# Performance work log

Hardware: AMD Instinct MI355X
Metric: run time of the kernel (lower is better)

The kernel has to match this reference:

```python
import jax, jax.numpy as jnp
import numpy as np

B, N, L, H = 8, 2048, 1280, 160
GAMMA = 1.0  # fixed buffer, gamma_init_value=1, not trainable


def setup_inputs() -> dict:
    key = jax.random.key(0)
    ks = jax.random.split(key, 7)
    s_in = 1.0 / np.sqrt(L)  # conv1d default init scale (approx; randn used for testing)
    return {
        "x": jax.random.normal(ks[0], (B, N, L), dtype=jnp.float32),
        "Wq": jax.random.normal(ks[1], (H, L), dtype=jnp.float32) * s_in,
        "bq": jax.random.normal(ks[2], (H,), dtype=jnp.float32) * s_in,
        "Wk": jax.random.normal(ks[3], (H, L), dtype=jnp.float32) * s_in,
        "bk": jax.random.normal(ks[4], (H,), dtype=jnp.float32) * s_in,
        "Wv": jax.random.normal(ks[5], (L, L), dtype=jnp.float32) * s_in,
        "bv": jax.random.normal(ks[6], (L,), dtype=jnp.float32) * s_in,
    }


def reference(x, Wq, bq, Wk, bk, Wv, bv):
    # 1x1 Conv1d on x.permute(0,2,1) == per-token linear projection
    q = jnp.einsum("bnl,hl->bnh", x, Wq) + bq          # [B,N,H]
    k = jnp.einsum("bnl,hl->bnh", x, Wk) + bk          # [B,N,H]
    v = jnp.einsum("bnl,ml->bnm", x, Wv) + bv          # [B,N,L]
    energy = jnp.einsum("bih,bjh->bij", q, k)          # [B,N,N]
    attn = jax.nn.softmax(energy, axis=-1)
    out = jnp.einsum("bij,bjm->bim", attn, v)          # [B,N,L]
    return GAMMA * out + x                              # [B,N,L]
```

## Files before the change

kernel.cpp:

```cpp
#include <hip/hip_runtime.h>

#define BB 8
#define NN 2048
#define LL 1280
#define HH 160
#define BN (BB*NN)
#define NO (2*HH + LL)
#define SHIFT 40.0f

typedef __attribute__((ext_vector_type(8))) short short8;
typedef __attribute__((ext_vector_type(4))) float floatx4;

__device__ __forceinline__ unsigned short f2bf(float f) {
    unsigned int u = __builtin_bit_cast(unsigned int, f);
    u = (u + 0x7FFFu + ((u >> 16) & 1u)) >> 16;
    return (unsigned short)u;
}
__device__ __forceinline__ float bf2f(unsigned short h) {
    unsigned int u = ((unsigned int)h) << 16;
    return __builtin_bit_cast(float, u);
}
__device__ __forceinline__ void split2(float f, unsigned short& hi, unsigned short& lo) {
    hi = f2bf(f);
    lo = f2bf(f - bf2f(hi));
}


__device__ __forceinline__ void gl16(const unsigned short* g, unsigned short* l) {
    __builtin_amdgcn_global_load_lds(
        (const __attribute__((address_space(1))) unsigned int*)g,
        (__attribute__((address_space(3))) unsigned int*)l, 16, 0, 0);
}

__global__ __launch_bounds__(256) void cast_w(
    const float* __restrict__ Wq, const float* __restrict__ Wk, const float* __restrict__ Wv,
    unsigned short* __restrict__ wqk_h, unsigned short* __restrict__ wqk_l,
    unsigned short* __restrict__ wv)
{
    int o = blockIdx.x;
    if (o < 2*HH) {
        const float* src = (o < HH) ? (Wq + (size_t)o * LL) : (Wk + (size_t)(o - HH) * LL);
        unsigned short* dh = wqk_h + (size_t)o * LL;
        unsigned short* dl = wqk_l + (size_t)o * LL;
        for (int c = threadIdx.x; c < LL; c += 256) {
            unsigned short h, l;
            split2(src[c], h, l);
            dh[c] = h; dl[c] = l;
        }
    } else {
        int f = o - 2*HH;
        const float* src = Wv + (size_t)f * LL;
        unsigned short* dstF = wv + (size_t)(f >> 4) * 20480 + (f & 15) * 8;
        for (int c = threadIdx.x * 4; c < LL; c += 256 * 4) {
            float4 v = *(const float4*)(src + c);
            ushort4 u;
            u.x = f2bf(v.x); u.y = f2bf(v.y); u.z = f2bf(v.z); u.w = f2bf(v.w);
            *(ushort4*)(dstF + (size_t)(c >> 5) * 512 + ((c >> 3) & 3) * 128 + (c & 7)) = u;
        }
    }
}

__global__ __launch_bounds__(256) void cast_x(
    const float* __restrict__ x, unsigned short* __restrict__ xh)
{
    const int g   = blockIdx.x;
    const int tid = threadIdx.x;
    const float* src = x + (size_t)(g * 16 + (tid & 15)) * LL + ((tid >> 4) & 3) * 8;
    unsigned short* dst = xh + (size_t)g * 20480 + tid * 8;
    const int ks0 = tid >> 6;
    #pragma unroll
    for (int it = 0; it < 10; it++) {
        int k0 = (it * 4 + ks0) * 32;
        float4 f0 = *(const float4*)(src + k0);
        float4 f1 = *(const float4*)(src + k0 + 4);
        short8 h8;
        h8[0]=(short)f2bf(f0.x); h8[1]=(short)f2bf(f0.y); h8[2]=(short)f2bf(f0.z); h8[3]=(short)f2bf(f0.w);
        h8[4]=(short)f2bf(f1.x); h8[5]=(short)f2bf(f1.y); h8[6]=(short)f2bf(f1.z); h8[7]=(short)f2bf(f1.w);
        *(short8*)(dst + it * 2048) = h8;
    }
}

__global__ __launch_bounds__(256, 2) void proj_qk(
    const float* __restrict__ x,
    const unsigned short* __restrict__ wh, const unsigned short* __restrict__ wl,
    const float* __restrict__ bq, const float* __restrict__ bk,
    unsigned short* __restrict__ qh, unsigned short* __restrict__ ql,
    unsigned short* __restrict__ kh, unsigned short* __restrict__ kl)
{
    __shared__ __align__(16) unsigned short Ah[128 * 40];
    __shared__ __align__(16) unsigned short Al[128 * 40];
    __shared__ __align__(16) unsigned short Bh[64 * 40];
    __shared__ __align__(16) unsigned short Bl[64 * 40];

    const int o0 = blockIdx.x * 64;
    const int m0 = blockIdx.y * 128;
    const int tid = threadIdx.x;
    const int wave = tid >> 6, lane = tid & 63;
    const int l15 = lane & 15, l4 = lane >> 4;

    floatx4 acc[2][4] = {};

    const int sr = tid >> 2;
    const int sc = (tid & 3) * 8;

    for (int k0 = 0; k0 < LL; k0 += 32) {
        __syncthreads();
        #pragma unroll
        for (int h = 0; h < 2; h++) {
            int r = sr + h * 64;
            const float* xp = x + (size_t)(m0 + r) * LL + k0 + sc;
            float4 f0 = *(const float4*)xp;
            float4 f1 = *(const float4*)(xp + 4);
            float fv[8] = {f0.x, f0.y, f0.z, f0.w, f1.x, f1.y, f1.z, f1.w};
            short8 h8, l8;
            #pragma unroll
            for (int i = 0; i < 8; i++) {
                unsigned short hh, lll;
                split2(fv[i], hh, lll);
                h8[i] = (short)hh; l8[i] = (short)lll;
            }
            *(short8*)&Ah[r * 40 + sc] = h8;
            *(short8*)&Al[r * 40 + sc] = l8;
        }
        *(short8*)&Bh[sr * 40 + sc] = *(const short8*)&wh[(size_t)(o0 + sr) * LL + k0 + sc];
        *(short8*)&Bl[sr * 40 + sc] = *(const short8*)&wl[(size_t)(o0 + sr) * LL + k0 + sc];
        __syncthreads();

        short8 ah0 = *(const short8*)&Ah[(wave * 32 + l15) * 40 + l4 * 8];
        short8 ah1 = *(const short8*)&Ah[(wave * 32 + 16 + l15) * 40 + l4 * 8];
        short8 al0 = *(const short8*)&Al[(wave * 32 + l15) * 40 + l4 * 8];
        short8 al1 = *(const short8*)&Al[(wave * 32 + 16 + l15) * 40 + l4 * 8];
        #pragma unroll
        for (int ct = 0; ct < 4; ct++) {
            short8 bh8 = *(const short8*)&Bh[(ct * 16 + l15) * 40 + l4 * 8];
            short8 bl8 = *(const short8*)&Bl[(ct * 16 + l15) * 40 + l4 * 8];
            acc[0][ct] = __builtin_amdgcn_mfma_f32_16x16x32_bf16(ah0, bh8, acc[0][ct], 0, 0, 0);
            acc[0][ct] = __builtin_amdgcn_mfma_f32_16x16x32_bf16(al0, bh8, acc[0][ct], 0, 0, 0);
            acc[0][ct] = __builtin_amdgcn_mfma_f32_16x16x32_bf16(ah0, bl8, acc[0][ct], 0, 0, 0);
            acc[1][ct] = __builtin_amdgcn_mfma_f32_16x16x32_bf16(ah1, bh8, acc[1][ct], 0, 0, 0);
            acc[1][ct] = __builtin_amdgcn_mfma_f32_16x16x32_bf16(al1, bh8, acc[1][ct], 0, 0, 0);
            acc[1][ct] = __builtin_amdgcn_mfma_f32_16x16x32_bf16(ah1, bl8, acc[1][ct], 0, 0, 0);
        }
    }

    #pragma unroll
    for (int rt = 0; rt < 2; rt++)
        #pragma unroll
        for (int ct = 0; ct < 4; ct++)
            #pragma unroll
            for (int r = 0; r < 4; r++) {
                int m = m0 + wave * 32 + rt * 16 + l4 * 4 + r;
                int o = o0 + ct * 16 + l15;
                float val = acc[rt][ct][r] + ((o < HH) ? bq[o] : bk[o - HH]);
                unsigned short vh, vl;
                split2(val, vh, vl);
                int oo = (o < HH) ? o : (o - HH);
                size_t fa = (size_t)(m >> 4) * 2560 + (oo >> 5) * 512
                          + ((oo >> 3) & 3) * 128 + (m & 15) * 8 + (oo & 7);
                if (o < HH) {
                    qh[fa] = vh;
                    ql[fa] = vl;
                } else {
                    kh[fa] = vh;
                    kl[fa] = vl;
                }
            }
}

__global__ __launch_bounds__(256, 3) void proj_v(
    const unsigned short* __restrict__ xh, const unsigned short* __restrict__ wv,
    const float* __restrict__ bv, unsigned short* __restrict__ vt)
{
    __shared__ __align__(16) unsigned short Sm[3 * 8192];

    const int bid = blockIdx.x;
    const int xcd = bid & 7;
    const int q   = bid >> 3;
    const int mt  = xcd * 16 + q / 10;
    const int ft  = q % 10;
    const int m0 = mt * 128;
    const int f0 = ft * 128;

    const int tid = threadIdx.x;
    const int wave = tid >> 6, lane = tid & 63;
    const int l15 = lane & 15, l4 = lane >> 4;
    const int wm = wave >> 1, wn = wave & 1;

    const unsigned short* AF = xh + (size_t)(m0 >> 4) * 20480;
    const unsigned short* BF = wv + (size_t)(f0 >> 4) * 20480;

    const int sp0 = tid, sp1 = 256 + tid;
    const unsigned sa0 = (unsigned)(sp0 >> 6) * 20480u + (sp0 & 63) * 8;
    const unsigned sa1 = (unsigned)(sp1 >> 6) * 20480u + (sp1 & 63) * 8;

    floatx4 acc[4][4] = {};

    auto STAGE = [&](int slot, int ks) {
        unsigned short* A  = Sm + slot * 8192;
        unsigned short* Bs = A + 4096;
        const unsigned ko = (unsigned)ks * 512u;
        gl16(AF + sa0 + ko, A  + sp0 * 8);
        gl16(BF + sa0 + ko, Bs + sp0 * 8);
        gl16(AF + sa1 + ko, A  + sp1 * 8);
        gl16(BF + sa1 + ko, Bs + sp1 * 8);
    };

    auto COMPUTE = [&](int slot) {
        const unsigned short* A  = Sm + slot * 8192;
        const unsigned short* Bs = A + 4096;
        short8 a[4], bb[4];
        #pragma unroll
        for (int mf = 0; mf < 4; mf++)
            a[mf] = *(const short8*)(A + ((wm * 4 + mf) * 64 + lane) * 8);
        #pragma unroll
        for (int nf = 0; nf < 4; nf++)
            bb[nf] = *(const short8*)(Bs + ((wn * 4 + nf) * 64 + lane) * 8);
        __builtin_amdgcn_s_setprio(1);
        #pragma unroll
        for (int mf = 0; mf < 4; mf++)
            #pragma unroll
            for (int nf = 0; nf < 4; nf++)
                acc[mf][nf] = __builtin_amdgcn_mfma_f32_16x16x32_bf16(a[mf], bb[nf], acc[mf][nf], 0, 0, 0);
        __builtin_amdgcn_s_setprio(0);
    };

    STAGE(0, 0); STAGE(1, 1); STAGE(2, 2);

    int s = 0;
    for (int kt = 0; kt < 37; ++kt) {
        asm volatile("s_waitcnt vmcnt(8)" ::: "memory");
        asm volatile("s_barrier" ::: "memory");
        COMPUTE(s);
        asm volatile("s_barrier" ::: "memory");
        STAGE(s, kt + 3);
        s = (s == 2) ? 0 : s + 1;
    }
    asm volatile("s_waitcnt vmcnt(8)" ::: "memory");
    asm volatile("s_barrier" ::: "memory");
    COMPUTE(s); s = (s == 2) ? 0 : s + 1;
    asm volatile("s_waitcnt vmcnt(4)" ::: "memory");
    asm volatile("s_barrier" ::: "memory");
    COMPUTE(s); s = (s == 2) ? 0 : s + 1;
    asm volatile("s_waitcnt vmcnt(0)" ::: "memory");
    asm volatile("s_barrier" ::: "memory");
    COMPUTE(s);

    const int b    = m0 >> 11;
    const int tokb = (m0 & 2047) + wm * 64;
    unsigned short* vtB = vt + (size_t)b * LL * NN;
    float bvv[4];
    #pragma unroll
    for (int nf = 0; nf < 4; nf++)
        bvv[nf] = bv[f0 + wn * 64 + nf * 16 + l15];

    #pragma unroll
    for (int mf = 0; mf < 4; mf++)
        #pragma unroll
        for (int nf = 0; nf < 4; nf++) {
            int f   = f0 + wn * 64 + nf * 16 + l15;
            int tok = tokb + mf * 16 + l4 * 4;
            ushort4 u;
            u.x = f2bf(acc[mf][nf][0] + bvv[nf]);
            u.y = f2bf(acc[mf][nf][1] + bvv[nf]);
            u.z = f2bf(acc[mf][nf][2] + bvv[nf]);
            u.w = f2bf(acc[mf][nf][3] + bvv[nf]);
            *(ushort4*)(vtB + (size_t)(f >> 4) * 32768 + (tok >> 5) * 512
                        + ((tok >> 3) & 3) * 128 + (f & 15) * 8 + (tok & 7)) = u;
        }
}

__global__ __launch_bounds__(256, 2) void s_exp(
    const unsigned short* __restrict__ qhp, const unsigned short* __restrict__ qlp,
    const unsigned short* __restrict__ khp, const unsigned short* __restrict__ klp,
    unsigned short* __restrict__ P, float* __restrict__ Lsum)
{
    __shared__ float sums[4][32];
    const int b  = blockIdx.y;
    const int i0 = blockIdx.x * 32;
    const int tid = threadIdx.x;
    const int wave = tid >> 6, lane = tid & 63;
    const int l15 = lane & 15, l4 = lane >> 4;

    short8 aqh[2][5], aql[2][5];
    #pragma unroll
    for (int rt = 0; rt < 2; rt++) {
        const size_t rowb = (size_t)((b * NN + i0 + rt * 16) >> 4) * 2560 + lane * 8;
        #pragma unroll
        for (int ks = 0; ks < 5; ks++) {
            aqh[rt][ks] = *(const short8*)&qhp[rowb + ks * 512];
            aql[rt][ks] = *(const short8*)&qlp[rowb + ks * 512];
        }
    }

    float sr[2][4] = {};
    unsigned short* Pb = P + (size_t)b * NN * NN + (size_t)(i0 >> 4) * 32768;

    for (int c0 = 0; c0 < NN; c0 += 256) {
        const int jb = c0 + wave * 64;
        #pragma unroll
        for (int ct = 0; ct < 4; ct++) {
            const int tok0 = jb + ct * 16;
            const int tok  = tok0 + l15;
            const size_t kbase = (size_t)((b * NN + tok0) >> 4) * 2560 + lane * 8;
            floatx4 a0[3] = {{0,0,0,0},{0,0,0,0},{0,0,0,0}};
            floatx4 a1[3] = {{0,0,0,0},{0,0,0,0},{0,0,0,0}};
            #pragma unroll
            for (int ks = 0; ks < 5; ks++) {
                short8 bh = *(const short8*)&khp[kbase + ks * 512];
                short8 bl = *(const short8*)&klp[kbase + ks * 512];
                a0[0] = __builtin_amdgcn_mfma_f32_16x16x32_bf16(aqh[0][ks], bh, a0[0], 0, 0, 0);
                a0[1] = __builtin_amdgcn_mfma_f32_16x16x32_bf16(aql[0][ks], bh, a0[1], 0, 0, 0);
                a0[2] = __builtin_amdgcn_mfma_f32_16x16x32_bf16(aqh[0][ks], bl, a0[2], 0, 0, 0);
                a1[0] = __builtin_amdgcn_mfma_f32_16x16x32_bf16(aqh[1][ks], bh, a1[0], 0, 0, 0);
                a1[1] = __builtin_amdgcn_mfma_f32_16x16x32_bf16(aql[1][ks], bh, a1[1], 0, 0, 0);
                a1[2] = __builtin_amdgcn_mfma_f32_16x16x32_bf16(aqh[1][ks], bl, a1[2], 0, 0, 0);
            }
            const size_t tbase = (size_t)(tok >> 5) * 512 + ((tok >> 3) & 3) * 128 + (tok & 7);
            #pragma unroll
            for (int r = 0; r < 4; r++) {
                float e0 = a0[0][r] + a0[1][r] + a0[2][r];
                float e1 = a1[0][r] + a1[1][r] + a1[2][r];
                unsigned short pb0 = f2bf(__expf(e0 - SHIFT));
                unsigned short pb1 = f2bf(__expf(e1 - SHIFT));
                Pb[tbase + (l4 * 4 + r) * 8] = pb0;
                Pb[tbase + (l4 * 4 + r) * 8 + 32768] = pb1;
                sr[0][r] += bf2f(pb0);
                sr[1][r] += bf2f(pb1);
            }
        }
    }

    #pragma unroll
    for (int rt = 0; rt < 2; rt++)
        #pragma unroll
        for (int r = 0; r < 4; r++) {
            float v = sr[rt][r];
            v += __shfl_xor(v, 1);
            v += __shfl_xor(v, 2);
            v += __shfl_xor(v, 4);
            v += __shfl_xor(v, 8);
            if (l15 == 0) sums[wave][rt * 16 + l4 * 4 + r] = v;
        }
    __syncthreads();
    if (tid < 32)
        Lsum[(size_t)b * NN + i0 + tid] =
            sums[0][tid] + sums[1][tid] + sums[2][tid] + sums[3][tid];
}

__global__ __launch_bounds__(256, 3) void pv_gemm(
    const unsigned short* __restrict__ P, const unsigned short* __restrict__ vt,
    const float* __restrict__ Lsum,
    const float* __restrict__ x, float* __restrict__ out)
{
    __shared__ __align__(16) unsigned short Sm[3 * 8192];

    const int p0 = blockIdx.x;
    const int b  = p0 & 7;
    const int t  = p0 >> 3;
    const int n0 = (t % 10) * 128;
    const int m0 = (t / 10) * 128;

    const int tid = threadIdx.x;
    const int wave = tid >> 6, lane = tid & 63;
    const int l15 = lane & 15, l4 = lane >> 4;
    const int wm = wave >> 1, wn = wave & 1;

    const unsigned short* PbF = P  + (size_t)b * NN * NN + (size_t)(m0 >> 4) * 32768;
    const unsigned short* VbF = vt + (size_t)b * LL * NN + (size_t)(n0 >> 4) * 32768;

    const int sp0 = tid, sp1 = 256 + tid;
    const unsigned sa0 = (unsigned)(sp0 >> 6) * 32768u + (sp0 & 63) * 8;
    const unsigned sa1 = (unsigned)(sp1 >> 6) * 32768u + (sp1 & 63) * 8;

    floatx4 acc[4][4] = {};

    auto STAGE = [&](int slot, int ks) {
        unsigned short* A  = Sm + slot * 8192;
        unsigned short* Bs = A + 4096;
        const unsigned ko = (unsigned)ks * 512u;
        gl16(PbF + sa0 + ko, A  + sp0 * 8);
        gl16(VbF + sa0 + ko, Bs + sp0 * 8);
        gl16(PbF + sa1 + ko, A  + sp1 * 8);
        gl16(VbF + sa1 + ko, Bs + sp1 * 8);
    };

    auto COMPUTE = [&](int slot) {
        const unsigned short* A  = Sm + slot * 8192;
        const unsigned short* Bs = A + 4096;
        short8 a[4], bb[4];
        #pragma unroll
        for (int mf = 0; mf < 4; mf++)
            a[mf] = *(const short8*)(A + ((wm * 4 + mf) * 64 + lane) * 8);
        #pragma unroll
        for (int nf = 0; nf < 4; nf++)
            bb[nf] = *(const short8*)(Bs + ((wn * 4 + nf) * 64 + lane) * 8);
        __builtin_amdgcn_s_setprio(1);
        #pragma unroll
        for (int mf = 0; mf < 4; mf++)
            #pragma unroll
            for (int nf = 0; nf < 4; nf++)
                acc[mf][nf] = __builtin_amdgcn_mfma_f32_16x16x32_bf16(a[mf], bb[nf], acc[mf][nf], 0, 0, 0);
        __builtin_amdgcn_s_setprio(0);
    };

    STAGE(0, 0); STAGE(1, 1); STAGE(2, 2);

    int s = 0;
    for (int kt = 0; kt < 61; ++kt) {
        asm volatile("s_waitcnt vmcnt(8)" ::: "memory");
        asm volatile("s_barrier" ::: "memory");
        COMPUTE(s);
        asm volatile("s_barrier" ::: "memory");
        STAGE(s, kt + 3);
        s = (s == 2) ? 0 : s + 1;
    }
    asm volatile("s_waitcnt vmcnt(8)" ::: "memory");
    asm volatile("s_barrier" ::: "memory");
    COMPUTE(s); s = (s == 2) ? 0 : s + 1;
    asm volatile("s_waitcnt vmcnt(4)" ::: "memory");
    asm volatile("s_barrier" ::: "memory");
    COMPUTE(s); s = (s == 2) ? 0 : s + 1;
    asm volatile("s_waitcnt vmcnt(0)" ::: "memory");
    asm volatile("s_barrier" ::: "memory");
    COMPUTE(s);

    float linv[4][4];
    #pragma unroll
    for (int mf = 0; mf < 4; mf++)
        #pragma unroll
        for (int r = 0; r < 4; r++)
            linv[mf][r] = 1.0f / Lsum[(size_t)b * NN + m0 + wm * 64 + mf * 16 + l4 * 4 + r];

    #pragma unroll
    for (int mf = 0; mf < 4; mf++)
        #pragma unroll
        for (int nf = 0; nf < 4; nf++)
            #pragma unroll
            for (int r = 0; r < 4; r++) {
                int row = m0 + wm * 64 + mf * 16 + l4 * 4 + r;
                int col = n0 + wn * 64 + nf * 16 + l15;
                size_t idx = ((size_t)b * NN + row) * LL + col;
                out[idx] = acc[mf][nf][r] * linv[mf][r] + x[idx];
            }
}

extern "C" void kernel_launch(void* const* d_in, const int* in_sizes, int n_in,
                              void* d_out, int out_size, void* d_ws, size_t ws_size,
                              hipStream_t stream) {
    const float* x  = (const float*)d_in[0];
    const float* Wq = (const float*)d_in[1];
    const float* bq = (const float*)d_in[2];
    const float* Wk = (const float*)d_in[3];
    const float* bk = (const float*)d_in[4];
    const float* Wv = (const float*)d_in[5];
    const float* bv = (const float*)d_in[6];
    float* out = (float*)d_out;

    unsigned short* wqk_h = (unsigned short*)d_ws;
    unsigned short* wqk_l = wqk_h + (size_t)2*HH * LL;
    unsigned short* wv    = wqk_l + (size_t)2*HH * LL;
    unsigned short* qh    = wv    + (size_t)LL * LL;
    unsigned short* ql    = qh    + (size_t)BN * HH;
    unsigned short* kh    = ql    + (size_t)BN * HH;
    unsigned short* kl    = kh    + (size_t)BN * HH;
    unsigned short* vt    = kl    + (size_t)BN * HH;
    unsigned short* P     = vt    + (size_t)BB * LL * NN;
    float*          Lsum  = (float*)(P + (size_t)BB * NN * NN);
    unsigned short* xh    = P;

    cast_w<<<dim3(NO), dim3(256), 0, stream>>>(Wq, Wk, Wv, wqk_h, wqk_l, wv);

    cast_x<<<dim3(BN / 16), dim3(256), 0, stream>>>(x, xh);

    dim3 gqk(2*HH / 64, BN / 128);
    proj_qk<<<gqk, dim3(256), 0, stream>>>(x, wqk_h, wqk_l, bq, bk, qh, ql, kh, kl);

    proj_v<<<dim3(1280), dim3(256), 0, stream>>>(xh, wv, bv, vt);

    dim3 gs(NN / 32, BB);
    s_exp<<<gs, dim3(256), 0, stream>>>(qh, ql, kh, kl, P, Lsum);

    pv_gemm<<<dim3(1280), dim3(256), 0, stream>>>(P, vt, Lsum, x, out);
}
```

Measured before the change: 479.2 us.

## Precompute x hi/lo bf16 split and restructure QK projection without LDS

cast_x now writes both the high and low bf16 parts of x in MFMA fragment layout, into a buffer that aliases vt. cast_w writes the Wq/Wk hi/lo parts in the same fragment layout. proj_qk is rewritten so each block covers 64 rows against all 320 Q/K outputs, loading fragments straight from global memory with no LDS staging or barriers. This removes the old behaviour of re-reading fp32 x and redoing the hi/lo split once per 64-column output block. The cost is an extra xl buffer write and every wave re-reading the shared A fragments from cache.

```diff
diff --git a/kernel.cpp b/kernel.cpp
--- a/kernel.cpp
+++ b/kernel.cpp
@@ -40,12 +40,13 @@
     int o = blockIdx.x;
     if (o < 2*HH) {
         const float* src = (o < HH) ? (Wq + (size_t)o * LL) : (Wk + (size_t)(o - HH) * LL);
-        unsigned short* dh = wqk_h + (size_t)o * LL;
-        unsigned short* dl = wqk_l + (size_t)o * LL;
+        unsigned short* dh = wqk_h + (size_t)(o >> 4) * 20480 + (o & 15) * 8;
+        unsigned short* dl = wqk_l + (size_t)(o >> 4) * 20480 + (o & 15) * 8;
         for (int c = threadIdx.x; c < LL; c += 256) {
             unsigned short h, l;
             split2(src[c], h, l);
-            dh[c] = h; dl[c] = l;
+            unsigned off = (unsigned)(c >> 5) * 512 + ((c >> 3) & 3) * 128 + (c & 7);
+            dh[off] = h; dl[off] = l;
         }
     } else {
         int f = o - 2*HH;
@@ -61,110 +62,96 @@
 }
 
 __global__ __launch_bounds__(256) void cast_x(
-    const float* __restrict__ x, unsigned short* __restrict__ xh)
+    const float* __restrict__ x,
+    unsigned short* __restrict__ xh, unsigned short* __restrict__ xl)
 {
     const int g   = blockIdx.x;
     const int tid = threadIdx.x;
     const float* src = x + (size_t)(g * 16 + (tid & 15)) * LL + ((tid >> 4) & 3) * 8;
-    unsigned short* dst = xh + (size_t)g * 20480 + tid * 8;
+    unsigned short* dsth = xh + (size_t)g * 20480 + tid * 8;
+    unsigned short* dstl = xl + (size_t)g * 20480 + tid * 8;
     const int ks0 = tid >> 6;
     #pragma unroll
     for (int it = 0; it < 10; it++) {
         int k0 = (it * 4 + ks0) * 32;
         float4 f0 = *(const float4*)(src + k0);
         float4 f1 = *(const float4*)(src + k0 + 4);
-        short8 h8;
-        h8[0]=(short)f2bf(f0.x); h8[1]=(short)f2bf(f0.y); h8[2]=(short)f2bf(f0.z); h8[3]=(short)f2bf(f0.w);
-        h8[4]=(short)f2bf(f1.x); h8[5]=(short)f2bf(f1.y); h8[6]=(short)f2bf(f1.z); h8[7]=(short)f2bf(f1.w);
-        *(short8*)(dst + it * 2048) = h8;
+        float fv[8] = {f0.x, f0.y, f0.z, f0.w, f1.x, f1.y, f1.z, f1.w};
+        short8 h8, l8;
+        #pragma unroll
+        for (int i = 0; i < 8; i++) {
+            unsigned short hh, lll;
+            split2(fv[i], hh, lll);
+            h8[i] = (short)hh; l8[i] = (short)lll;
+        }
+        *(short8*)(dsth + it * 2048) = h8;
+        *(short8*)(dstl + it * 2048) = l8;
     }
 }
 
 __global__ __launch_bounds__(256, 2) void proj_qk(
-    const float* __restrict__ x,
+    const unsigned short* __restrict__ xh, const unsigned short* __restrict__ xl,
     const unsigned short* __restrict__ wh, const unsigned short* __restrict__ wl,
     const float* __restrict__ bq, const float* __restrict__ bk,
     unsigned short* __restrict__ qh, unsigned short* __restrict__ ql,
     unsigned short* __restrict__ kh, unsigned short* __restrict__ kl)
 {
-    __shared__ __align__(16) unsigned short Ah[128 * 40];
-    __shared__ __align__(16) unsigned short Al[128 * 40];
-    __shared__ __align__(16) unsigned short Bh[64 * 40];
-    __shared__ __align__(16) unsigned short Bl[64 * 40];
-
-    const int o0 = blockIdx.x * 64;
-    const int m0 = blockIdx.y * 128;
+    const int mg0 = blockIdx.x * 4;
     const int tid = threadIdx.x;
     const int wave = tid >> 6, lane = tid & 63;
     const int l15 = lane & 15, l4 = lane >> 4;
 
-    floatx4 acc[2][4] = {};
-
-    const int sr = tid >> 2;
-    const int sc = (tid & 3) * 8;
-
-    for (int k0 = 0; k0 < LL; k0 += 32) {
-        __syncthreads();
-        #pragma unroll
-        for (int h = 0; h < 2; h++) {
-            int r = sr + h * 64;
-            const float* xp = x + (size_t)(m0 + r) * LL + k0 + sc;
-            float4 f0 = *(const float4*)xp;
-            float4 f1 = *(const float4*)(xp + 4);
-            float fv[8] = {f0.x, f0.y, f0.z, f0.w, f1.x, f1.y, f1.z, f1.w};
-            short8 h8, l8;
-            #pragma unroll
-            for (int i = 0; i < 8; i++) {
-                unsigned short hh, lll;
-                split2(fv[i], hh, lll);
-                h8[i] = (short)hh; l8[i] = (short)lll;
+    const unsigned aBase = (unsigned)mg0 * 20480u + lane * 8;
+    const unsigned bBase = (unsigned)(wave * 5) * 20480u + lane * 8;
+
+    floatx4 acc[4][5] = {};
+
+    #pragma unroll 2
+    for (int ks = 0; ks < 40; ks++) {
+        const unsigned ko = (unsigned)ks * 512u;
+        short8 ah[4], al[4], bh[5], bl[5];
+        #pragma unroll
+        for (int mf = 0; mf < 4; mf++) {
+            ah[mf] = *(const short8*)(xh + aBase + mf * 20480u + ko);
+            al[mf] = *(const short8*)(xl + aBase + mf * 20480u + ko);
+        }
+        #pragma unroll
+        for (int nf = 0; nf < 5; nf++) {
+            bh[nf] = *(const short8*)(wh + bBase + nf * 20480u + ko);
+            bl[nf] = *(const short8*)(wl + bBase + nf * 20480u + ko);
+        }
+        #pragma unroll
+        for (int mf = 0; mf < 4; mf++)
+            #pragma unroll
+            for (int nf = 0; nf < 5; nf++) {
+                acc[mf][nf] = __builtin_amdgcn_mfma_f32_16x16x32_bf16(ah[mf], bh[nf], acc[mf][nf], 0, 0, 0);
+                acc[mf][nf] = __builtin_amdgcn_mfma_f32_16x16x32_bf16(al[mf], bh[nf], acc[mf][nf], 0, 0, 0);
+                acc[mf][nf] = __builtin_amdgcn_mfma_f32_16x16x32_bf16(ah[mf], bl[nf], acc[mf][nf], 0, 0, 0);
             }
-            *(short8*)&Ah[r * 40 + sc] = h8;
-            *(short8*)&Al[r * 40 + sc] = l8;
-        }
-        *(short8*)&Bh[sr * 40 + sc] = *(const short8*)&wh[(size_t)(o0 + sr) * LL + k0 + sc];
-        *(short8*)&Bl[sr * 40 + sc] = *(const short8*)&wl[(size_t)(o0 + sr) * LL + k0 + sc];
-        __syncthreads();
-
-        short8 ah0 = *(const short8*)&Ah[(wave * 32 + l15) * 40 + l4 * 8];
-        short8 ah1 = *(const short8*)&Ah[(wave * 32 + 16 + l15) * 40 + l4 * 8];
-        short8 al0 = *(const short8*)&Al[(wave * 32 + l15) * 40 + l4 * 8];
-        short8 al1 = *(const short8*)&Al[(wave * 32 + 16 + l15) * 40 + l4 * 8];
-        #pragma unroll
-        for (int ct = 0; ct < 4; ct++) {
-            short8 bh8 = *(const short8*)&Bh[(ct * 16 + l15) * 40 + l4 * 8];
-            short8 bl8 = *(const short8*)&Bl[(ct * 16 + l15) * 40 + l4 * 8];
-            acc[0][ct] = __builtin_amdgcn_mfma_f32_16x16x32_bf16(ah0, bh8, acc[0][ct], 0, 0, 0);
-            acc[0][ct] = __builtin_amdgcn_mfma_f32_16x16x32_bf16(al0, bh8, acc[0][ct], 0, 0, 0);
-            acc[0][ct] = __builtin_amdgcn_mfma_f32_16x16x32_bf16(ah0, bl8, acc[0][ct], 0, 0, 0);
-            acc[1][ct] = __builtin_amdgcn_mfma_f32_16x16x32_bf16(ah1, bh8, acc[1][ct], 0, 0, 0);
-            acc[1][ct] = __builtin_amdgcn_mfma_f32_16x16x32_bf16(al1, bh8, acc[1][ct], 0, 0, 0);
-            acc[1][ct] = __builtin_amdgcn_mfma_f32_16x16x32_bf16(ah1, bl8, acc[1][ct], 0, 0, 0);
-        }
-    }
-
-    #pragma unroll
-    for (int rt = 0; rt < 2; rt++)
-        #pragma unroll
-        for (int ct = 0; ct < 4; ct++)
+    }
+
+    #pragma unroll
+    for (int nf = 0; nf < 5; nf++) {
+        int o = wave * 80 + nf * 16 + l15;
+        bool isQ = (o < HH);
+        float bias = isQ ? bq[o] : bk[o - HH];
+        int oo = isQ ? o : (o - HH);
+        unsigned short* dh = isQ ? qh : kh;
+        unsigned short* dl = isQ ? ql : kl;
+        unsigned ob = (unsigned)(oo >> 5) * 512u + ((oo >> 3) & 3) * 128u + (oo & 7);
+        #pragma unroll
+        for (int mf = 0; mf < 4; mf++) {
+            unsigned fa0 = (unsigned)(mg0 + mf) * 2560u + ob + (l4 * 4) * 8u;
             #pragma unroll
             for (int r = 0; r < 4; r++) {
-                int m = m0 + wave * 32 + rt * 16 + l4 * 4 + r;
-                int o = o0 + ct * 16 + l15;
-                float val = acc[rt][ct][r] + ((o < HH) ? bq[o] : bk[o - HH]);
+                float val = acc[mf][nf][r] + bias;
                 unsigned short vh, vl;
                 split2(val, vh, vl);
-                int oo = (o < HH) ? o : (o - HH);
-                size_t fa = (size_t)(m >> 4) * 2560 + (oo >> 5) * 512
-                          + ((oo >> 3) & 3) * 128 + (m & 15) * 8 + (oo & 7);
-                if (o < HH) {
-                    qh[fa] = vh;
-                    ql[fa] = vl;
-                } else {
-                    kh[fa] = vh;
-                    kl[fa] = vl;
-                }
+                dh[fa0 + r * 8] = vh;
+                dl[fa0 + r * 8] = vl;
             }
+        }
+    }
 }
 
 __global__ __launch_bounds__(256, 3) void proj_v(
@@ -467,13 +454,14 @@
     unsigned short* P     = vt    + (size_t)BB * LL * NN;
     float*          Lsum  = (float*)(P + (size_t)BB * NN * NN);
     unsigned short* xh    = P;
+    unsigned short* xl    = vt;
 
     cast_w<<<dim3(NO), dim3(256), 0, stream>>>(Wq, Wk, Wv, wqk_h, wqk_l, wv);
 
-    cast_x<<<dim3(BN / 16), dim3(256), 0, stream>>>(x, xh);
-
-    dim3 gqk(2*HH / 64, BN / 128);
-    proj_qk<<<gqk, dim3(256), 0, stream>>>(x, wqk_h, wqk_l, bq, bk, qh, ql, kh, kl);
+    cast_x<<<dim3(BN / 16), dim3(256), 0, stream>>>(x, xh, xl);
+
+    proj_qk<<<dim3(BN / 64), dim3(256), 0, stream>>>(
+        xh, xl, wqk_h, wqk_l, bq, bk, qh, ql, kh, kl);
 
     proj_v<<<dim3(1280), dim3(256), 0, stream>>>(xh, wv, bv, vt);
 
```

New measurement: 479.8 us. Within noise of the previous version (+0.1%).
